# Performance work log

Measured on AMD Instinct MI355X. Metric: run time of the kernel, lower is better.

## Reference

```python
import jax, jax.numpy as jnp
import numpy as np

N_QUBITS = 14
N_LAYERS = 4
N_CLASSES = 10
BATCH = 1024


def apply_1q(state, gate, wire):
    """Apply a 2x2 gate ([2,2] shared or [B,2,2] batched) to `wire` of state [B,2,...,2]."""
    s = jnp.moveaxis(state, wire + 1, -1)
    shp = s.shape
    s = s.reshape(shp[0], -1, 2)
    if gate.ndim == 3:
        s = jnp.einsum('bij,bkj->bki', gate, s)
    else:
        s = jnp.einsum('ij,bkj->bki', gate, s)
    return jnp.moveaxis(s.reshape(shp), -1, wire + 1)


def apply_cnot(state, c, t):
    s = jnp.moveaxis(state, (c + 1, t + 1), (-2, -1))
    s = jnp.stack([s[..., 0, :], s[..., 1, ::-1]], axis=-2)
    return jnp.moveaxis(s, (-2, -1), (c + 1, t + 1))


def simulate(x, q_params):
    """Batched statevector sim of: RY(x_i) embed -> BasicEntanglerLayers(RX + CNOT ring) -> <Z_i>."""
    B, n = x.shape
    state = jnp.zeros((B,) + (2,) * n, jnp.complex64)
    state = state.at[(slice(None),) + (0,) * n].set(1.0)

    # RY(x_i) on each wire (angles batched per sample)
    c, s = jnp.cos(0.5 * x), jnp.sin(0.5 * x)
    for w in range(n):
        g = jnp.stack([jnp.stack([c[:, w], -s[:, w]], -1),
                       jnp.stack([s[:, w], c[:, w]], -1)], -2).astype(jnp.complex64)  # [B,2,2]
        state = apply_1q(state, g, w)

    # BasicEntanglerLayers: per layer RX(weights[l,i]) on every wire, then CNOT ring
    cw, sw = jnp.cos(0.5 * q_params), jnp.sin(0.5 * q_params)
    n_layers = q_params.shape[0]
    for l in range(n_layers):
        for w in range(n):
            cc = cw[l, w].astype(jnp.complex64)
            isw = (-1j) * sw[l, w].astype(jnp.complex64)
            g = jnp.stack([jnp.stack([cc, isw]), jnp.stack([isw, cc])])  # [2,2] RX
            state = apply_1q(state, g, w)
        if n == 2:
            state = apply_cnot(state, 0, 1)
        else:
            for w in range(n):
                state = apply_cnot(state, w, (w + 1) % n)

    # <Z_i> = P(bit_i=0) - P(bit_i=1)
    p = jnp.abs(state) ** 2  # [B,2,...,2] real
    axes_all = tuple(range(1, n + 1))
    z = []
    for w in range(n):
        pw = jnp.sum(p, axis=tuple(a for a in axes_all if a != w + 1))  # [B,2]
        z.append(pw[:, 0] - pw[:, 1])
    return jnp.stack(z, -1).astype(jnp.float32)  # [B, n]


def setup_inputs() -> dict:
    key = jax.random.key(0)
    k1, k2, k3, k4 = jax.random.split(key, 4)
    x = jax.random.normal(k1, (BATCH, N_QUBITS), dtype=jnp.float32)
    q_params = 0.01 * jax.random.normal(k2, (N_LAYERS, N_QUBITS), dtype=jnp.float32)
    fc_w = jax.random.normal(k3, (N_CLASSES, N_QUBITS), dtype=jnp.float32) / np.sqrt(N_QUBITS)
    fc_b = jax.random.normal(k4, (N_CLASSES,), dtype=jnp.float32) * 0.01
    return {"x": x, "q_params": q_params, "fc_w": fc_w, "fc_b": fc_b}


def reference(x, q_params, fc_w, fc_b):
    q_out = simulate(x, q_params)            # [B, n_qubits]
    logits = q_out @ fc_w.T + fc_b           # [B, n_classes]
    return logits
```

## Files before the change

### kernel.cpp

```cpp
#include <hip/hip_runtime.h>
#include <hip/hip_fp16.h>
#include <math.h>


#define NQ 14
#define NLAYERS 4
#define NCLASSES 10
#define BLOCK 512

typedef _Float16 f16;
typedef _Float16 f16x2 __attribute__((ext_vector_type(2)));
typedef _Float16 f16x8 __attribute__((ext_vector_type(8)));
typedef _Float16 f16x4 __attribute__((ext_vector_type(4)));
typedef float f32x4 __attribute__((ext_vector_type(4)));
typedef unsigned int u32;
typedef u32 u32x2 __attribute__((ext_vector_type(2)));

__device__ __forceinline__ f32x4 mf(f16x8 a, f16x8 b, f32x4 c) {
  return __builtin_amdgcn_mfma_f32_16x16x32_f16(a, b, c, 0, 0, 0);
}
__device__ __forceinline__ int swz(int t) { return ((t ^ (t >> 3)) & 7) << 3; }

__device__ __forceinline__ f16x4 cvt4(f32x4 v) {
  u32x2 r;
  r[0] = __builtin_bit_cast(u32, __builtin_amdgcn_cvt_pkrtz(v[0], v[1]));
  r[1] = __builtin_bit_cast(u32, __builtin_amdgcn_cvt_pkrtz(v[2], v[3]));
  return __builtin_bit_cast(f16x4, r);
}

__device__ __forceinline__ int finv5(int n) {
  n ^= ((n >> 3) & 1) << 4;
  n ^= ((n >> 2) & 1) << 3;
  n ^= ((n >> 1) & 1) << 2;
  n ^= (n & 1) << 1;
  return n;
}
__device__ __forceinline__ int finv3(int n) {
  n ^= ((n >> 2) & 1) << 3;
  n ^= ((n >> 1) & 1) << 2;
  n ^= (n & 1) << 1;
  return n;
}

__device__ __forceinline__ void build32(f16* Bc, const float* qc, const float* qs,
                                        int base, int tid) {
  const float c0 = qc[base], c1 = qc[base+1], c2 = qc[base+2], c3 = qc[base+3], c4 = qc[base+4];
  const float s0 = qs[base], s1 = qs[base+1], s2 = qs[base+2], s3 = qs[base+3], s4 = qs[base+4];
#pragma unroll
  for (int e = tid; e < 1024; e += BLOCK) {
    const int n = e >> 5, k = e & 31;
    const int d = finv5(n) ^ k;
    float mag = ((d & 1) ? s0 : c0) * ((d & 2) ? s1 : c1);
    mag *= ((d & 4) ? s2 : c2) * ((d & 8) ? s3 : c3);
    mag *= ((d & 16) ? s4 : c4);
    const int t = __popc(d) & 3;
    const f16 v = (f16)((t == 1 || t == 2) ? -mag : mag);
    const int p = 256 * (k >> 3) + 8 * n + (k & 7);
    const bool isreal = !(t & 1);
    Bc[p]        = isreal ? v : (f16)0.f;
    Bc[p + 1024] = isreal ? (f16)0.f : v;
  }
}
__device__ __forceinline__ void buildC(f16* Bc, const float* qc, const float* qs,
                                       int base, int tid) {
  const float c0 = qc[base], c1 = qc[base+1], c2 = qc[base+2], c3 = qc[base+3];
  const float s0 = qs[base], s1 = qs[base+1], s2 = qs[base+2], s3 = qs[base+3];
  const int n = tid >> 5, k = tid & 31;
  f16 vr = (f16)0.f, vi = (f16)0.f;
  if (k < 16) {
    const int d = finv3(n) ^ k;
    float mag = ((d & 1) ? s0 : c0) * ((d & 2) ? s1 : c1);
    mag *= ((d & 4) ? s2 : c2) * ((d & 8) ? s3 : c3);
    const int t = __popc(d) & 3;
    const f16 v = (f16)((t == 1 || t == 2) ? -mag : mag);
    if (t & 1) vi = v; else vr = v;
  }
  const int p = 256 * (k >> 3) + 8 * n + (k & 7);
  Bc[p]        = vr;
  Bc[p + 1024] = vi;
}

template<bool CTRL, bool STORE_C>
__device__ __forceinline__ void pass32(f16* __restrict__ reP, f16* __restrict__ imP,
                                       const f16* __restrict__ BcR, int tid) {
  const int lane = tid & 63, wave = tid >> 6;
  const int q = lane >> 4, cc = lane & 15;
  int n0 = cc, n1 = cc | 16;
  if (CTRL && wave >= 4) { n0 ^= 31; n1 ^= 31; }
  const f16x8 br0 = *(const f16x8*)(BcR + 256 * q + 8 * n0);
  const f16x8 bi0 = *(const f16x8*)(BcR + 1024 + 256 * q + 8 * n0);
  const f16x8 br1 = *(const f16x8*)(BcR + 256 * q + 8 * n1);
  const f16x8 bi1 = *(const f16x8*)(BcR + 1024 + 256 * q + 8 * n1);
  f16x4 outR[8], outI[8];
#pragma unroll
  for (int i = 0; i < 4; ++i) {
    const int mt = wave * 4 + i;
    const int pA = mt * 512 + ((128 * q + 8 * cc) ^ swz(mt));
    const f16x8 Ar = *(const f16x8*)(reP + pA);
    const f16x8 Ai = *(const f16x8*)(imP + pA);
    const f16x8 nAi = -Ai;
    {
      f32x4 aR = {0.f,0.f,0.f,0.f}, aI = {0.f,0.f,0.f,0.f};
      aR = mf(Ar, br0, aR); aR = mf(nAi, bi0, aR);
      aI = mf(Ar, bi0, aI); aI = mf(Ai, br0, aI);
      outR[i * 2 + 0] = cvt4(aR);
      outI[i * 2 + 0] = cvt4(aI);
    }
    {
      f32x4 aR = {0.f,0.f,0.f,0.f}, aI = {0.f,0.f,0.f,0.f};
      aR = mf(Ar, br1, aR); aR = mf(nAi, bi1, aR);
      aI = mf(Ar, bi1, aI); aI = mf(Ai, br1, aI);
      outR[i * 2 + 1] = cvt4(aR);
      outI[i * 2 + 1] = cvt4(aI);
    }
  }
  __syncthreads();
#pragma unroll
  for (int i = 0; i < 4; ++i) {
    const int mt = wave * 4 + i;
#pragma unroll
    for (int nt = 0; nt < 2; ++nt) {
      const int n5 = nt * 16 + cc;
      int pS;
      if constexpr (STORE_C) {
        const int tC = (mt >> 4) + 2 * n5;
        pS = tC * 256 + ((128 * (q >> 1) + 8 * (mt & 15) + 4 * (q & 1)) ^ swz(tC));
      } else {
        pS = n5 * 512 + ((128 * (2 * (mt & 1) + (q >> 1)) + 8 * (mt >> 1) + 4 * (q & 1)) ^ swz(n5));
      }
      *(f16x4*)(reP + pS) = outR[i * 2 + nt];
      *(f16x4*)(imP + pS) = outI[i * 2 + nt];
    }
  }
}

template<bool FINAL>
__device__ __forceinline__ void passC(f16* __restrict__ reP, f16* __restrict__ imP,
                                      const f16* __restrict__ BcR, int tid,
                                      float* __restrict__ zloc) {
  const int lane = tid & 63, wave = tid >> 6;
  const int q = lane >> 4, cc = lane & 15;
  int n0 = cc;
  if (wave >= 4) n0 ^= 15;
  const f16x8 br = *(const f16x8*)(BcR + 256 * q + 8 * n0);
  const f16x8 bi = *(const f16x8*)(BcR + 1024 + 256 * q + 8 * n0);
  f16x4 outR[8], outI[8];
#pragma unroll
  for (int i = 0; i < 8; ++i) {
    const int mtC = wave * 8 + i;
    const int pA = mtC * 256 + ((128 * (q & 1) + 8 * cc) ^ swz(mtC));
    const f16x8 Ar = *(const f16x8*)(reP + pA);
    const f16x8 Ai = *(const f16x8*)(imP + pA);
    const f16x8 nAi = -Ai;
    f32x4 aR = {0.f,0.f,0.f,0.f}, aI = {0.f,0.f,0.f,0.f};
    aR = mf(Ar, br, aR); aR = mf(nAi, bi, aR);
    aI = mf(Ar, bi, aI); aI = mf(Ai, br, aI);
    if constexpr (FINAL) {
      float p0 = aR[0]*aR[0] + aI[0]*aI[0];
      float p1 = aR[1]*aR[1] + aI[1]*aI[1];
      float p2 = aR[2]*aR[2] + aI[2]*aI[2];
      float p3 = aR[3]*aR[3] + aI[3]*aI[3];
      if (cc & 8) { float t = p0; p0 = p1; p1 = t; t = p2; p2 = p3; p3 = t; }
      const float ps = p0 + p1 + p2 + p3;
      zloc[0] += (p0 - p1) + (p2 - p3);
      zloc[1] += (p0 + p1) - (p2 + p3);
      zloc[2] += (q & 1) ? -ps : ps;
      zloc[3] += (q & 2) ? -ps : ps;
#pragma unroll
      for (int w = 0; w < 6; ++w) zloc[4 + w] += ((mtC >> w) & 1) ? -ps : ps;
#pragma unroll
      for (int w = 0; w < 4; ++w) zloc[10 + w] += ((cc >> w) & 1) ? -ps : ps;
    } else {
      if (cc & 8) {
        f32x4 tR = aR, tI = aI;
        aR[0] = tR[1]; aR[1] = tR[0]; aR[2] = tR[3]; aR[3] = tR[2];
        aI[0] = tI[1]; aI[1] = tI[0]; aI[2] = tI[3]; aI[3] = tI[2];
      }
      outR[i] = cvt4(aR);
      outI[i] = cvt4(aI);
    }
  }
  if constexpr (!FINAL) {
    __syncthreads();
#pragma unroll
    for (int i = 0; i < 8; ++i) {
      const int mtC = wave * 8 + i;
      const int tP = 2 * cc + (mtC >> 5);
      const int pS = tP * 512 +
          ((128 * (2 * (mtC & 1) + (q >> 1)) + 8 * ((mtC >> 1) & 15) + 4 * (q & 1)) ^ swz(tP));
      *(f16x4*)(reP + pS) = outR[i];
      *(f16x4*)(imP + pS) = outI[i];
    }
  }
}

__global__ __launch_bounds__(BLOCK, 4) void qsim_kernel(
    const float* __restrict__ x, const float* __restrict__ qp,
    const float* __restrict__ fcw, const float* __restrict__ fcb,
    float* __restrict__ out) {
  extern __shared__ unsigned char smem[];
  f16* reP = (f16*)smem;
  f16* imP = reP + 16384;
  f16* Bc  = imP + 16384;
  float* qc = (float*)(Bc + 2048);
  float* qs = qc + 56;
  float* xc = qs + 56;
  float* xs = xc + 14;

  const int b = blockIdx.x;
  const int tid = threadIdx.x;

  if (tid < NQ) {
    float sv, cv; sincosf(0.5f * x[b * NQ + tid], &sv, &cv);
    xc[tid] = cv; xs[tid] = sv;
  } else if (tid >= 64 && tid < 64 + NLAYERS * NQ) {
    const int k = tid - 64;
    float sv, cv; sincosf(0.5f * qp[k], &sv, &cv);
    qc[k] = cv; qs[k] = sv;
  }
  __syncthreads();

  float* Flo  = (float*)Bc;
  float* psi  = Flo + 32;
  float* PsiR = psi + 32;
  float* PsiI = PsiR + 32;
  if (tid < 32) {
    float f = 1.f;
#pragma unroll
    for (int j = 0; j < 5; ++j) f *= ((tid >> j) & 1) ? xs[5 + j] : xc[5 + j];
    Flo[tid] = f;
  } else if (tid < 64) {
    const int k = tid - 32;
    float f = 1.f;
#pragma unroll
    for (int j = 0; j < 5; ++j) f *= ((k >> j) & 1) ? xs[j] : xc[j];
    psi[k] = f;
  }
  __syncthreads();
  if (tid < 32) {
    const float c0 = qc[0], c1 = qc[1], c2 = qc[2], c3 = qc[3], c4 = qc[4];
    const float s0 = qs[0], s1 = qs[1], s2 = qs[2], s3 = qs[3], s4 = qs[4];
    const int a = finv5(tid);
    float ar = 0.f, ai = 0.f;
    for (int k = 0; k < 32; ++k) {
      const int d = a ^ k;
      float mag = ((d & 1) ? s0 : c0) * ((d & 2) ? s1 : c1);
      mag *= ((d & 4) ? s2 : c2) * ((d & 8) ? s3 : c3);
      mag *= ((d & 16) ? s4 : c4);
      mag *= psi[k];
      const int t = __popc(d) & 3;
      if (t == 0) ar += mag; else if (t == 1) ai -= mag;
      else if (t == 2) ar -= mag; else ai += mag;
    }
    PsiR[tid] = ar; PsiI[tid] = ai;
  }
  __syncthreads();
  {
    float fhi = 1.f;
#pragma unroll
    for (int j = 0; j < 4; ++j) fhi *= ((tid >> j) & 1) ? xs[10 + j] : xc[10 + j];
    const float cr = fhi * PsiR[tid >> 4], ci = fhi * PsiI[tid >> 4];
    const int t = tid >> 4;
    const int sz = swz(t);
    float Fl[32];
#pragma unroll
    for (int j = 0; j < 32; ++j) Fl[j] = Flo[j];
    __syncthreads();
#pragma unroll
    for (int kb = 0; kb < 4; ++kb) {
      f16x8 hr, hi;
#pragma unroll
      for (int j = 0; j < 8; ++j) {
        const float F = Fl[8 * kb + j];
        hr[j] = (f16)(F * cr);
        hi[j] = (f16)(F * ci);
      }
      const int pb = t * 512 + ((128 * kb + 8 * (tid & 15)) ^ sz);
      *(f16x8*)(reP + pb) = hr;
      *(f16x8*)(imP + pb) = hi;
    }
  }
  build32(Bc, qc, qs, 0 * NQ + 5, tid);
  __syncthreads();

  pass32<true, true>(reP, imP, Bc, tid);          __syncthreads();
  buildC(Bc, qc, qs, 0 * NQ + 10, tid);           __syncthreads();
  passC<false>(reP, imP, Bc, tid, nullptr);       __syncthreads();
#pragma unroll
  for (int l = 1; l < NLAYERS; ++l) {
    build32(Bc, qc, qs, l * NQ + 0, tid);         __syncthreads();
    pass32<false, false>(reP, imP, Bc, tid);      __syncthreads();
    build32(Bc, qc, qs, l * NQ + 5, tid);         __syncthreads();
    pass32<true, true>(reP, imP, Bc, tid);        __syncthreads();
    buildC(Bc, qc, qs, l * NQ + 10, tid);         __syncthreads();
    if (l < NLAYERS - 1) {
      passC<false>(reP, imP, Bc, tid, nullptr);   __syncthreads();
    }
  }

  float zloc[NQ];
#pragma unroll
  for (int w = 0; w < NQ; ++w) zloc[w] = 0.f;
  passC<true>(reP, imP, Bc, tid, zloc);
  __syncthreads();

  float* zpart = (float*)Bc;
  float* zbuf  = zpart + 112;
#pragma unroll
  for (int w = 0; w < NQ; ++w) {
#pragma unroll
    for (int off = 32; off > 0; off >>= 1)
      zloc[w] += __shfl_down(zloc[w], off, 64);
  }
  const int wave = tid >> 6, lane = tid & 63;
  if (lane == 0) {
#pragma unroll
    for (int w = 0; w < NQ; ++w) zpart[wave * NQ + w] = zloc[w];
  }
  __syncthreads();
  if (tid < NQ) {
    float a = 0.f;
#pragma unroll
    for (int v = 0; v < 8; ++v) a += zpart[v * NQ + tid];
    zbuf[tid] = a;
  }
  __syncthreads();
  if (tid < NCLASSES) {
    float acc = fcb[tid];
#pragma unroll
    for (int w = 0; w < NQ; ++w) acc = fmaf(zbuf[w], fcw[tid * NQ + w], acc);
    out[b * NCLASSES + tid] = acc;
  }
}

extern "C" void kernel_launch(void* const* d_in, const int* in_sizes, int n_in,
                              void* d_out, int out_size, void* d_ws, size_t ws_size,
                              hipStream_t stream) {
  const float* x   = (const float*)d_in[0];
  const float* qp  = (const float*)d_in[1];
  const float* fcw = (const float*)d_in[2];
  const float* fcb = (const float*)d_in[3];
  float* out = (float*)d_out;
  const int B = in_sizes[0] / NQ;

  const size_t shmem = (size_t)(2 * 16384 + 2048) * sizeof(f16)
                     + (size_t)(56 + 56 + 14 + 14) * sizeof(float);
  (void)hipFuncSetAttribute((const void*)qsim_kernel,
                            hipFuncAttributeMaxDynamicSharedMemorySize, (int)shmem);
  qsim_kernel<<<B, BLOCK, shmem, stream>>>(x, qp, fcw, fcb, out);
}
```

Baseline: 139.7 us.

## Double-buffer state and gate matrices in LDS, use 1024-thread blocks

Keeps two copies of the statevector and two gate-matrix buffers in shared memory, so each pass reads one buffer and writes the other. This removes the mid-pass barrier and lets the next gate matrix be built while the current pass runs, roughly halving the barriers. The block grows from 512 to 1024 threads so each wave handles half as many tiles. In exchange shared memory per block about doubles (~136KB), which limits how many blocks fit on a CU and may lower occupancy.

After: 158.1 us. 1.13x slower.

```diff
diff --git a/kernel.cpp b/kernel.cpp
--- a/kernel.cpp
+++ b/kernel.cpp
@@ -6,10 +6,9 @@
 #define NQ 14
 #define NLAYERS 4
 #define NCLASSES 10
-#define BLOCK 512
+#define BLOCK 1024
 
 typedef _Float16 f16;
-typedef _Float16 f16x2 __attribute__((ext_vector_type(2)));
 typedef _Float16 f16x8 __attribute__((ext_vector_type(8)));
 typedef _Float16 f16x4 __attribute__((ext_vector_type(4)));
 typedef float f32x4 __attribute__((ext_vector_type(4)));
@@ -46,9 +45,8 @@
                                         int base, int tid) {
   const float c0 = qc[base], c1 = qc[base+1], c2 = qc[base+2], c3 = qc[base+3], c4 = qc[base+4];
   const float s0 = qs[base], s1 = qs[base+1], s2 = qs[base+2], s3 = qs[base+3], s4 = qs[base+4];
-#pragma unroll
-  for (int e = tid; e < 1024; e += BLOCK) {
-    const int n = e >> 5, k = e & 31;
+  if (tid < 1024) {
+    const int n = tid >> 5, k = tid & 31;
     const int d = finv5(n) ^ k;
     float mag = ((d & 1) ? s0 : c0) * ((d & 2) ? s1 : c1);
     mag *= ((d & 4) ? s2 : c2) * ((d & 8) ? s3 : c3);
@@ -65,61 +63,49 @@
                                        int base, int tid) {
   const float c0 = qc[base], c1 = qc[base+1], c2 = qc[base+2], c3 = qc[base+3];
   const float s0 = qs[base], s1 = qs[base+1], s2 = qs[base+2], s3 = qs[base+3];
-  const int n = tid >> 5, k = tid & 31;
-  f16 vr = (f16)0.f, vi = (f16)0.f;
-  if (k < 16) {
-    const int d = finv3(n) ^ k;
-    float mag = ((d & 1) ? s0 : c0) * ((d & 2) ? s1 : c1);
-    mag *= ((d & 4) ? s2 : c2) * ((d & 8) ? s3 : c3);
-    const int t = __popc(d) & 3;
-    const f16 v = (f16)((t == 1 || t == 2) ? -mag : mag);
-    if (t & 1) vi = v; else vr = v;
-  }
-  const int p = 256 * (k >> 3) + 8 * n + (k & 7);
-  Bc[p]        = vr;
-  Bc[p + 1024] = vi;
+  if (tid < 512) {
+    const int n = tid >> 5, k = tid & 31;
+    f16 vr = (f16)0.f, vi = (f16)0.f;
+    if (k < 16) {
+      const int d = finv3(n) ^ k;
+      float mag = ((d & 1) ? s0 : c0) * ((d & 2) ? s1 : c1);
+      mag *= ((d & 4) ? s2 : c2) * ((d & 8) ? s3 : c3);
+      const int t = __popc(d) & 3;
+      const f16 v = (f16)((t == 1 || t == 2) ? -mag : mag);
+      if (t & 1) vi = v; else vr = v;
+    }
+    const int p = 256 * (k >> 3) + 8 * n + (k & 7);
+    Bc[p]        = vr;
+    Bc[p + 1024] = vi;
+  }
 }
 
 template<bool CTRL, bool STORE_C>
-__device__ __forceinline__ void pass32(f16* __restrict__ reP, f16* __restrict__ imP,
+__device__ __forceinline__ void pass32(const f16* __restrict__ sRe, const f16* __restrict__ sIm,
+                                       f16* __restrict__ dRe, f16* __restrict__ dIm,
                                        const f16* __restrict__ BcR, int tid) {
   const int lane = tid & 63, wave = tid >> 6;
   const int q = lane >> 4, cc = lane & 15;
   int n0 = cc, n1 = cc | 16;
-  if (CTRL && wave >= 4) { n0 ^= 31; n1 ^= 31; }
+  if (CTRL && wave >= 8) { n0 ^= 31; n1 ^= 31; }
   const f16x8 br0 = *(const f16x8*)(BcR + 256 * q + 8 * n0);
   const f16x8 bi0 = *(const f16x8*)(BcR + 1024 + 256 * q + 8 * n0);
   const f16x8 br1 = *(const f16x8*)(BcR + 256 * q + 8 * n1);
   const f16x8 bi1 = *(const f16x8*)(BcR + 1024 + 256 * q + 8 * n1);
-  f16x4 outR[8], outI[8];
-#pragma unroll
-  for (int i = 0; i < 4; ++i) {
-    const int mt = wave * 4 + i;
+#pragma unroll
+  for (int i = 0; i < 2; ++i) {
+    const int mt = wave * 2 + i;
     const int pA = mt * 512 + ((128 * q + 8 * cc) ^ swz(mt));
-    const f16x8 Ar = *(const f16x8*)(reP + pA);
-    const f16x8 Ai = *(const f16x8*)(imP + pA);
+    const f16x8 Ar = *(const f16x8*)(sRe + pA);
+    const f16x8 Ai = *(const f16x8*)(sIm + pA);
     const f16x8 nAi = -Ai;
-    {
+#pragma unroll
+    for (int nt = 0; nt < 2; ++nt) {
+      const f16x8 br = nt ? br1 : br0;
+      const f16x8 bi = nt ? bi1 : bi0;
       f32x4 aR = {0.f,0.f,0.f,0.f}, aI = {0.f,0.f,0.f,0.f};
-      aR = mf(Ar, br0, aR); aR = mf(nAi, bi0, aR);
-      aI = mf(Ar, bi0, aI); aI = mf(Ai, br0, aI);
-      outR[i * 2 + 0] = cvt4(aR);
-      outI[i * 2 + 0] = cvt4(aI);
-    }
-    {
-      f32x4 aR = {0.f,0.f,0.f,0.f}, aI = {0.f,0.f,0.f,0.f};
-      aR = mf(Ar, br1, aR); aR = mf(nAi, bi1, aR);
-      aI = mf(Ar, bi1, aI); aI = mf(Ai, br1, aI);
-      outR[i * 2 + 1] = cvt4(aR);
-      outI[i * 2 + 1] = cvt4(aI);
-    }
-  }
-  __syncthreads();
-#pragma unroll
-  for (int i = 0; i < 4; ++i) {
-    const int mt = wave * 4 + i;
-#pragma unroll
-    for (int nt = 0; nt < 2; ++nt) {
+      aR = mf(Ar, br, aR); aR = mf(nAi, bi, aR);
+      aI = mf(Ar, bi, aI); aI = mf(Ai, br, aI);
       const int n5 = nt * 16 + cc;
       int pS;
       if constexpr (STORE_C) {
@@ -128,29 +114,29 @@
       } else {
         pS = n5 * 512 + ((128 * (2 * (mt & 1) + (q >> 1)) + 8 * (mt >> 1) + 4 * (q & 1)) ^ swz(n5));
       }
-      *(f16x4*)(reP + pS) = outR[i * 2 + nt];
-      *(f16x4*)(imP + pS) = outI[i * 2 + nt];
+      *(f16x4*)(dRe + pS) = cvt4(aR);
+      *(f16x4*)(dIm + pS) = cvt4(aI);
     }
   }
 }
 
 template<bool FINAL>
-__device__ __forceinline__ void passC(f16* __restrict__ reP, f16* __restrict__ imP,
+__device__ __forceinline__ void passC(const f16* __restrict__ sRe, const f16* __restrict__ sIm,
+                                      f16* __restrict__ dRe, f16* __restrict__ dIm,
                                       const f16* __restrict__ BcR, int tid,
                                       float* __restrict__ zloc) {
   const int lane = tid & 63, wave = tid >> 6;
   const int q = lane >> 4, cc = lane & 15;
   int n0 = cc;
-  if (wave >= 4) n0 ^= 15;
+  if (wave >= 8) n0 ^= 15;
   const f16x8 br = *(const f16x8*)(BcR + 256 * q + 8 * n0);
   const f16x8 bi = *(const f16x8*)(BcR + 1024 + 256 * q + 8 * n0);
-  f16x4 outR[8], outI[8];
-#pragma unroll
-  for (int i = 0; i < 8; ++i) {
-    const int mtC = wave * 8 + i;
+#pragma unroll
+  for (int i = 0; i < 4; ++i) {
+    const int mtC = wave * 4 + i;
     const int pA = mtC * 256 + ((128 * (q & 1) + 8 * cc) ^ swz(mtC));
-    const f16x8 Ar = *(const f16x8*)(reP + pA);
-    const f16x8 Ai = *(const f16x8*)(imP + pA);
+    const f16x8 Ar = *(const f16x8*)(sRe + pA);
+    const f16x8 Ai = *(const f16x8*)(sIm + pA);
     const f16x8 nAi = -Ai;
     f32x4 aR = {0.f,0.f,0.f,0.f}, aI = {0.f,0.f,0.f,0.f};
     aR = mf(Ar, br, aR); aR = mf(nAi, bi, aR);
@@ -176,20 +162,11 @@
         aR[0] = tR[1]; aR[1] = tR[0]; aR[2] = tR[3]; aR[3] = tR[2];
         aI[0] = tI[1]; aI[1] = tI[0]; aI[2] = tI[3]; aI[3] = tI[2];
       }
-      outR[i] = cvt4(aR);
-      outI[i] = cvt4(aI);
-    }
-  }
-  if constexpr (!FINAL) {
-    __syncthreads();
-#pragma unroll
-    for (int i = 0; i < 8; ++i) {
-      const int mtC = wave * 8 + i;
       const int tP = 2 * cc + (mtC >> 5);
       const int pS = tP * 512 +
           ((128 * (2 * (mtC & 1) + (q >> 1)) + 8 * ((mtC >> 1) & 15) + 4 * (q & 1)) ^ swz(tP));
-      *(f16x4*)(reP + pS) = outR[i];
-      *(f16x4*)(imP + pS) = outI[i];
+      *(f16x4*)(dRe + pS) = cvt4(aR);
+      *(f16x4*)(dIm + pS) = cvt4(aI);
     }
   }
 }
@@ -199,10 +176,13 @@
     const float* __restrict__ fcw, const float* __restrict__ fcb,
     float* __restrict__ out) {
   extern __shared__ unsigned char smem[];
-  f16* reP = (f16*)smem;
-  f16* imP = reP + 16384;
-  f16* Bc  = imP + 16384;
-  float* qc = (float*)(Bc + 2048);
+  f16* S0re = (f16*)smem;
+  f16* S0im = S0re + 16384;
+  f16* S1re = S0im + 16384;
+  f16* S1im = S1re + 16384;
+  f16* Bc0  = S1im + 16384;
+  f16* Bc1  = Bc0 + 2048;
+  float* qc = (float*)(Bc1 + 2048);
   float* qs = qc + 56;
   float* xc = qs + 56;
   float* xs = xc + 14;
@@ -220,7 +200,7 @@
   }
   __syncthreads();
 
-  float* Flo  = (float*)Bc;
+  float* Flo  = (float*)Bc1;
   float* psi  = Flo + 32;
   float* PsiR = psi + 32;
   float* PsiI = PsiR + 32;
@@ -256,56 +236,59 @@
   }
   __syncthreads();
   {
+    const int u = tid >> 1, h = tid & 1;
     float fhi = 1.f;
 #pragma unroll
-    for (int j = 0; j < 4; ++j) fhi *= ((tid >> j) & 1) ? xs[10 + j] : xc[10 + j];
-    const float cr = fhi * PsiR[tid >> 4], ci = fhi * PsiI[tid >> 4];
-    const int t = tid >> 4;
+    for (int j = 0; j < 4; ++j) fhi *= ((u >> j) & 1) ? xs[10 + j] : xc[10 + j];
+    const float cr = fhi * PsiR[u >> 4], ci = fhi * PsiI[u >> 4];
+    const int t = u >> 4;
+    const int mlow = u & 15;
     const int sz = swz(t);
-    float Fl[32];
-#pragma unroll
-    for (int j = 0; j < 32; ++j) Fl[j] = Flo[j];
-    __syncthreads();
-#pragma unroll
-    for (int kb = 0; kb < 4; ++kb) {
+#pragma unroll
+    for (int kb = 0; kb < 2; ++kb) {
       f16x8 hr, hi;
 #pragma unroll
       for (int j = 0; j < 8; ++j) {
-        const float F = Fl[8 * kb + j];
+        const float F = Flo[16 * h + 8 * kb + j];
         hr[j] = (f16)(F * cr);
         hi[j] = (f16)(F * ci);
       }
-      const int pb = t * 512 + ((128 * kb + 8 * (tid & 15)) ^ sz);
-      *(f16x8*)(reP + pb) = hr;
-      *(f16x8*)(imP + pb) = hi;
-    }
-  }
-  build32(Bc, qc, qs, 0 * NQ + 5, tid);
-  __syncthreads();
-
-  pass32<true, true>(reP, imP, Bc, tid);          __syncthreads();
-  buildC(Bc, qc, qs, 0 * NQ + 10, tid);           __syncthreads();
-  passC<false>(reP, imP, Bc, tid, nullptr);       __syncthreads();
-#pragma unroll
-  for (int l = 1; l < NLAYERS; ++l) {
-    build32(Bc, qc, qs, l * NQ + 0, tid);         __syncthreads();
-    pass32<false, false>(reP, imP, Bc, tid);      __syncthreads();
-    build32(Bc, qc, qs, l * NQ + 5, tid);         __syncthreads();
-    pass32<true, true>(reP, imP, Bc, tid);        __syncthreads();
-    buildC(Bc, qc, qs, l * NQ + 10, tid);         __syncthreads();
-    if (l < NLAYERS - 1) {
-      passC<false>(reP, imP, Bc, tid, nullptr);   __syncthreads();
-    }
-  }
+      const int pb = t * 512 + ((128 * (2 * h + kb) + 8 * mlow) ^ sz);
+      *(f16x8*)(S0re + pb) = hr;
+      *(f16x8*)(S0im + pb) = hi;
+    }
+  }
+  build32(Bc0, qc, qs, 0 * NQ + 5, tid);
+  __syncthreads();
+
+  pass32<true, true>(S0re, S0im, S1re, S1im, Bc0, tid);
+  buildC (Bc1, qc, qs, 0 * NQ + 10, tid);                 __syncthreads();
+  passC<false>(S1re, S1im, S0re, S0im, Bc1, tid, nullptr);
+  build32(Bc0, qc, qs, 1 * NQ + 0, tid);                  __syncthreads();
+  pass32<false, false>(S0re, S0im, S1re, S1im, Bc0, tid);
+  build32(Bc1, qc, qs, 1 * NQ + 5, tid);                  __syncthreads();
+  pass32<true, true>(S1re, S1im, S0re, S0im, Bc1, tid);
+  buildC (Bc0, qc, qs, 1 * NQ + 10, tid);                 __syncthreads();
+  passC<false>(S0re, S0im, S1re, S1im, Bc0, tid, nullptr);
+  build32(Bc1, qc, qs, 2 * NQ + 0, tid);                  __syncthreads();
+  pass32<false, false>(S1re, S1im, S0re, S0im, Bc1, tid);
+  build32(Bc0, qc, qs, 2 * NQ + 5, tid);                  __syncthreads();
+  pass32<true, true>(S0re, S0im, S1re, S1im, Bc0, tid);
+  buildC (Bc1, qc, qs, 2 * NQ + 10, tid);                 __syncthreads();
+  passC<false>(S1re, S1im, S0re, S0im, Bc1, tid, nullptr);
+  build32(Bc0, qc, qs, 3 * NQ + 0, tid);                  __syncthreads();
+  pass32<false, false>(S0re, S0im, S1re, S1im, Bc0, tid);
+  build32(Bc1, qc, qs, 3 * NQ + 5, tid);                  __syncthreads();
+  pass32<true, true>(S1re, S1im, S0re, S0im, Bc1, tid);
+  buildC (Bc0, qc, qs, 3 * NQ + 10, tid);                 __syncthreads();
 
   float zloc[NQ];
 #pragma unroll
   for (int w = 0; w < NQ; ++w) zloc[w] = 0.f;
-  passC<true>(reP, imP, Bc, tid, zloc);
-  __syncthreads();
-
-  float* zpart = (float*)Bc;
-  float* zbuf  = zpart + 112;
+  passC<true>(S0re, S0im, nullptr, nullptr, Bc0, tid, zloc);
+
+  float* zpart = (float*)Bc1;
+  float* zbuf  = zpart + 16 * NQ;
 #pragma unroll
   for (int w = 0; w < NQ; ++w) {
 #pragma unroll
@@ -321,7 +304,7 @@
   if (tid < NQ) {
     float a = 0.f;
 #pragma unroll
-    for (int v = 0; v < 8; ++v) a += zpart[v * NQ + tid];
+    for (int v = 0; v < 16; ++v) a += zpart[v * NQ + tid];
     zbuf[tid] = a;
   }
   __syncthreads();
@@ -343,7 +326,7 @@
   float* out = (float*)d_out;
   const int B = in_sizes[0] / NQ;
 
-  const size_t shmem = (size_t)(2 * 16384 + 2048) * sizeof(f16)
+  const size_t shmem = (size_t)(4 * 16384 + 2 * 2048) * sizeof(f16)
                      + (size_t)(56 + 56 + 14 + 14) * sizeof(float);
   (void)hipFuncSetAttribute((const void*)qsim_kernel,
                             hipFuncAttributeMaxDynamicSharedMemorySize, (int)shmem);
```
